# Kernel optimization log

Hardware: AMD Instinct MI355X
Metric: run time of the kernel (lower is better)

The kernel has to match this reference:

```python
import jax, jax.numpy as jnp
import numpy as np

B, C, H, W = 8, 256, 80, 80
NH, NP = 8, 4               # num_heads, num_points
CPH = C // NH               # channels per head


def conv1x1(x, w, b):
    # x: [B,Cin,H,W], w: [Cout,Cin], b: [Cout]
    return jnp.einsum('bchw,oc->bohw', x, w) + b[None, :, None, None]


def grid_sample_bilinear(img, grid):
    # img: [N,C,Hi,Wi], grid: [N,Hg,Wg,2] in [-1,1] (x,y), align_corners=True, zeros padding
    N, Cc, Hi, Wi = img.shape
    Hg, Wg = grid.shape[1], grid.shape[2]
    ix = (grid[..., 0] + 1.0) * 0.5 * (Wi - 1)
    iy = (grid[..., 1] + 1.0) * 0.5 * (Hi - 1)
    x0 = jnp.floor(ix); y0 = jnp.floor(iy)
    x1 = x0 + 1.0;      y1 = y0 + 1.0
    wx1 = ix - x0; wx0 = 1.0 - wx1
    wy1 = iy - y0; wy0 = 1.0 - wy1
    imf = img.reshape(N, Cc, Hi * Wi)

    def gather(xc, yc):
        valid = (xc >= 0) & (xc <= Wi - 1) & (yc >= 0) & (yc <= Hi - 1)
        xi = jnp.clip(xc, 0, Wi - 1).astype(jnp.int32)
        yi = jnp.clip(yc, 0, Hi - 1).astype(jnp.int32)
        idx = (yi * Wi + xi).reshape(N, 1, Hg * Wg)
        v = jnp.take_along_axis(imf, jnp.broadcast_to(idx, (N, Cc, Hg * Wg)), axis=2)
        v = v.reshape(N, Cc, Hg, Wg)
        return v * valid[:, None].astype(img.dtype)

    out = (gather(x0, y0) * (wx0 * wy0)[:, None]
           + gather(x1, y0) * (wx1 * wy0)[:, None]
           + gather(x0, y1) * (wx0 * wy1)[:, None]
           + gather(x1, y1) * (wx1 * wy1)[:, None])
    return out


def setup_inputs() -> dict:
    key = jax.random.key(0)
    ks = jax.random.split(key, 9)
    s = 1.0 / np.sqrt(C)
    x = jax.random.normal(ks[0], (B, C, H, W), dtype=jnp.float32)
    Wv = jax.random.normal(ks[1], (C, C), dtype=jnp.float32) * s
    bv = jnp.zeros((C,), dtype=jnp.float32)
    Woff = jax.random.normal(ks[2], (NH * NP * 2, C), dtype=jnp.float32) * 0.01
    boff = jax.random.normal(ks[3], (NH * NP * 2,), dtype=jnp.float32) * 0.01
    Wa = jax.random.normal(ks[4], (NH * NP, C), dtype=jnp.float32) * 0.01
    ba = jnp.full((NH * NP,), float(np.log(1.0 / NP)), dtype=jnp.float32)
    Wo = jax.random.normal(ks[5], (C, C), dtype=jnp.float32) * s
    bo = jnp.zeros((C,), dtype=jnp.float32)
    return {"x": x, "Wv": Wv, "bv": bv, "Woff": Woff, "boff": boff,
            "Wa": Wa, "ba": ba, "Wo": Wo, "bo": bo}


def reference(x, Wv, bv, Woff, boff, Wa, ba, Wo, bo):
    value = conv1x1(x, Wv, bv)                      # [B,C,H,W]
    offsets = conv1x1(x, Woff, boff)                # [B,NH*NP*2,H,W]
    attn = conv1x1(x, Wa, ba).reshape(B, NH, NP, H, W)
    attn = jax.nn.softmax(attn, axis=2)             # softmax over points

    gy, gx = jnp.meshgrid(jnp.linspace(-1.0, 1.0, H), jnp.linspace(-1.0, 1.0, W), indexing='ij')
    base_grid = jnp.stack((gx, gy), axis=-1)[None, None, None]          # [1,1,1,H,W,2]

    off = offsets.reshape(B, NH, NP, 2, H, W).transpose(0, 1, 2, 4, 5, 3)  # [B,NH,NP,H,W,2]
    grid = (base_grid + off).reshape(B * NH * NP, H, W, 2)

    v = value.reshape(B, NH, CPH, H, W)
    v = jnp.broadcast_to(v[:, :, None], (B, NH, NP, CPH, H, W)).reshape(B * NH * NP, CPH, H, W)

    sampled = grid_sample_bilinear(v, grid).reshape(B, NH, NP, CPH, H, W)
    weighted = (sampled * attn[:, :, :, None]).sum(axis=2)              # [B,NH,CPH,H,W]
    weighted = weighted.reshape(B, C, H, W)
    return conv1x1(weighted, Wo, bo) + x
```

## Files before the change

kernel.cpp:

```cpp
#include <hip/hip_runtime.h>
#include <cstddef>
#include <cstdint>

#define B_    8
#define C_    256
#define Himg  80
#define Wimg  80
#define HW_   6400
#define NH_   8
#define NP_   4
#define MPROJ 352

using bf16x8 = __attribute__((ext_vector_type(8))) short;
using f32x4  = __attribute__((ext_vector_type(4))) float;
using f16x8  = __attribute__((ext_vector_type(8))) _Float16;
using f16x4  = __attribute__((ext_vector_type(4))) _Float16;

__device__ __forceinline__ unsigned short f2bf(float f) {
    union { float f; uint32_t u; } v; v.f = f;
    uint32_t r = v.u + 0x7FFFu + ((v.u >> 16) & 1u);
    return (unsigned short)(r >> 16);
}
__device__ __forceinline__ float bf2f(unsigned short s) {
    union { uint32_t u; float f; } v; v.u = ((uint32_t)s) << 16;
    return v.f;
}

#define GLD16(gsrc, ldst) \
    __builtin_amdgcn_global_load_lds( \
        (const __attribute__((address_space(1))) unsigned int*)(gsrc), \
        (__attribute__((address_space(3))) unsigned int*)(ldst), 16, 0, 0)

__global__ __launch_bounds__(256) void prep_and_transpose(
        const float* __restrict__ Wv,  const float* __restrict__ bv,
        const float* __restrict__ Woff, const float* __restrict__ boff,
        const float* __restrict__ Wa,  const float* __restrict__ ba,
        const float* __restrict__ Wo,  const float* __restrict__ x,
        short* __restrict__ WcatBf, short* __restrict__ WoBf,
        float* __restrict__ bcat,   short* __restrict__ xT) {
    __shared__ float tile[64][68];
    const int bid = blockIdx.x;
    const int t = threadIdx.x;
    if (bid < 640) {
        int o = bid;
        if (o < 384) {
            const float* src = nullptr; float bias = 0.f;
            if (o < 256)      { src = Wv   + (size_t)o * 256;         bias = bv[o];         }
            else if (o < 320) { src = Woff + (size_t)(o - 256) * 256; bias = boff[o - 256]; }
            else if (o < 352) { src = Wa   + (size_t)(o - 320) * 256; bias = ba[o - 320];   }
            WcatBf[(size_t)o * 256 + t] = src ? (short)f2bf(src[t]) : (short)0;
            if (t == 0) bcat[o] = bias;
        } else {
            int oo = o - 384;
            WoBf[(size_t)oo * 256 + t] = (short)f2bf(Wo[(size_t)oo * 256 + t]);
        }
        return;
    }
    const int b2 = bid - 640;
    const int p0 = (b2 % 100) * 64;
    const int k0 = ((b2 / 100) & 3) * 64;
    const int b  = b2 / 400;
    const float* xb = x + ((size_t)b * C_ + k0) * HW_ + p0;
    #pragma unroll
    for (int r = 0; r < 4; ++r) {
        int kk = r * 16 + (t >> 4);
        int pp = (t & 15) * 4;
        float4 v = *(const float4*)(xb + (size_t)kk * HW_ + pp);
        *(float4*)&tile[kk][pp] = v;
    }
    __syncthreads();
    const int pp = t >> 2, kc = (t & 3) * 16;
    short tmp[16];
    #pragma unroll
    for (int i = 0; i < 16; ++i) tmp[i] = (short)f2bf(tile[kc + i][pp]);
    short* dst = xT + ((size_t)b * HW_ + p0 + pp) * 256 + k0 + kc;
    *(bf16x8*)dst       = *(bf16x8*)tmp;
    *(bf16x8*)(dst + 8) = *(bf16x8*)(tmp + 8);
}

#define PSTAGE(buf, k0)                                                         \
    _Pragma("unroll")                                                           \
    for (int q = 0; q < 4; ++q) {                                               \
        int i = wid * 4 + q;                                                    \
        int row = i * 8 + (lane >> 3);                                          \
        int sc  = (lane & 7) ^ (row & 7);                                       \
        GLD16(Wb  + (size_t)(o0 + row) * 256 + (k0) + sc * 8,                   \
              &lA[(buf)][i * 512]);                                             \
        GLD16(xTb + (size_t)(p0 + row) * 256 + (k0) + sc * 8,                   \
              &lB[(buf)][i * 512]);                                             \
    }

#define PCOMPUTE(buf)                                                           \
    _Pragma("unroll")                                                           \
    for (int kk = 0; kk < 2; ++kk) {                                            \
        bf16x8 af[4], bfr[4];                                                   \
        _Pragma("unroll")                                                       \
        for (int m = 0; m < 4; ++m) {                                           \
            int row = wo0 + m * 16 + (lane & 15);                               \
            int cph = (kk * 4 + (lane >> 4)) ^ (row & 7);                       \
            af[m] = *(const bf16x8*)&lA[(buf)][row * 64 + cph * 8];             \
        }                                                                       \
        _Pragma("unroll")                                                       \
        for (int nn = 0; nn < 4; ++nn) {                                        \
            int row = wp0 + nn * 16 + (lane & 15);                              \
            int cph = (kk * 4 + (lane >> 4)) ^ (row & 7);                       \
            bfr[nn] = *(const bf16x8*)&lB[(buf)][row * 64 + cph * 8];           \
        }                                                                       \
        _Pragma("unroll")                                                       \
        for (int m = 0; m < 4; ++m)                                             \
            _Pragma("unroll")                                                   \
            for (int nn = 0; nn < 4; ++nn)                                      \
                acc[m][nn] = __builtin_amdgcn_mfma_f32_16x16x32_bf16(           \
                    af[m], bfr[nn], acc[m][nn], 0, 0, 0);                       \
    }

__global__ __launch_bounds__(256) void gemm_proj_mfma(
        const short* __restrict__ Wb, const float* __restrict__ bcat,
        const short* __restrict__ xT,
        short* __restrict__ val, _Float16* __restrict__ meta) {
    __shared__ short lA[2][8192];
    __shared__ short lB[2][8192];
    const int n = blockIdx.x;
    const int w = (n & 7) * 150 + (n >> 3);
    const int b = w / 150;
    const int r150 = w % 150;
    const int o0 = (r150 % 3) * 128;
    const int p0 = (r150 / 3) * 128;
    const int t = threadIdx.x;
    const int wid = t >> 6, lane = t & 63;
    const int wo0 = (wid & 1) * 64, wp0 = (wid >> 1) * 64;
    const short* xTb = xT + (size_t)b * HW_ * 256;
    f32x4 acc[4][4] = {};

    PSTAGE(0, 0)
    #pragma unroll
    for (int kt = 0; kt < 4; ++kt) {
        const int cur = kt & 1;
        if (kt > 0) __builtin_amdgcn_s_barrier();
        if (kt < 3) { PSTAGE(cur ^ 1, (kt + 1) * 64) }
        if (kt < 3) { asm volatile("s_waitcnt vmcnt(8)" ::: "memory"); }
        else        { asm volatile("s_waitcnt vmcnt(0)" ::: "memory"); }
        __builtin_amdgcn_sched_barrier(0);
        __builtin_amdgcn_s_barrier();
        PCOMPUTE(cur)
    }

    #pragma unroll
    for (int m = 0; m < 4; ++m) {
        int oc = o0 + wo0 + m * 16 + (lane >> 4) * 4;
        if (oc >= MPROJ) continue;
        float4 bias = *(const float4*)(bcat + oc);
        #pragma unroll
        for (int nn = 0; nn < 4; ++nn) {
            int p = p0 + wp0 + nn * 16 + (lane & 15);
            f32x4 a = acc[m][nn];
            float v0 = a[0] + bias.x, v1 = a[1] + bias.y;
            float v2 = a[2] + bias.z, v3 = a[3] + bias.w;
            if (oc < 256) {
                int h = oc >> 5, c0 = oc & 31;
                ushort4 u;
                u.x = f2bf(v0); u.y = f2bf(v1); u.z = f2bf(v2); u.w = f2bf(v3);
                *(ushort4*)(val + (((size_t)(b * NH_ + h) * HW_) + p) * 32 + c0) = u;
            } else if (oc < 320) {
                f16x4 f;
                f[0] = (_Float16)(v0 * 39.5f); f[1] = (_Float16)(v1 * 39.5f);
                f[2] = (_Float16)(v2 * 39.5f); f[3] = (_Float16)(v3 * 39.5f);
                *(f16x4*)(meta + ((size_t)b * HW_ + p) * 96 + (oc - 256)) = f;
            } else {
                float mx = fmaxf(fmaxf(v0, v1), fmaxf(v2, v3));
                float e0 = __expf(v0 - mx), e1 = __expf(v1 - mx);
                float e2 = __expf(v2 - mx), e3 = __expf(v3 - mx);
                float inv = 1.f / (e0 + e1 + e2 + e3);
                f16x4 f;
                f[0] = (_Float16)(e0 * inv); f[1] = (_Float16)(e1 * inv);
                f[2] = (_Float16)(e2 * inv); f[3] = (_Float16)(e3 * inv);
                *(f16x4*)(meta + ((size_t)b * HW_ + p) * 96 + (oc - 256)) = f;
            }
        }
    }
}

__global__ __launch_bounds__(256) void sample_kern(
        const short* __restrict__ val, const _Float16* __restrict__ meta,
        short* __restrict__ wout) {
    const int t = threadIdx.x;
    const int wid = t >> 6, lane = t & 63;
    const int sub = lane >> 5, li = lane & 31;
    const int h = li >> 2, j = li & 3;
    const int orig = blockIdx.x;
    const int b = orig & 7;
    const int p = (orig >> 3) * 8 + wid * 2 + sub;
    const int yy = p / Wimg;
    const int xx = p - yy * Wimg;

    const _Float16* mrow = meta + ((size_t)b * HW_ + p) * 96;
    f16x4 w4 = *(const f16x4*)(mrow + 64 + h * 4);
    float wgt[4] = {(float)w4[0], (float)w4[1], (float)w4[2], (float)w4[3]};

    f16x8 off8 = *(const f16x8*)(mrow + h * 8);
    float ox[4] = {(float)off8[0], (float)off8[2], (float)off8[4], (float)off8[6]};
    float oy[4] = {(float)off8[1], (float)off8[3], (float)off8[5], (float)off8[7]};

    const short* vb = val + ((size_t)(b * NH_ + h) * HW_) * 32 + j * 8;

    float acc[8] = {};
    #pragma unroll
    for (int pt = 0; pt < NP_; ++pt) {
        float ix = (float)xx + ox[pt];
        float iy = (float)yy + oy[pt];
        float x0f = floorf(ix), y0f = floorf(iy);
        int   x0  = (int)x0f,   y0  = (int)y0f;
        float wx1 = ix - x0f, wx0 = 1.f - wx1;
        float wy1 = iy - y0f, wy0 = 1.f - wy1;
        int x0c = min(max(x0, 0), Wimg - 1), x1c = min(max(x0 + 1, 0), Wimg - 1);
        int y0c = min(max(y0, 0), Himg - 1), y1c = min(max(y0 + 1, 0), Himg - 1);
        float vx0 = (x0 >= 0 && x0 <= Wimg - 1)         ? wx0 : 0.f;
        float vx1 = (x0 + 1 >= 0 && x0 + 1 <= Wimg - 1) ? wx1 : 0.f;
        float vy0 = (y0 >= 0 && y0 <= Himg - 1)         ? wy0 : 0.f;
        float vy1 = (y0 + 1 >= 0 && y0 + 1 <= Himg - 1) ? wy1 : 0.f;
        bf16x8 u00 = *(const bf16x8*)(vb + (size_t)(y0c * Wimg + x0c) * 32);
        bf16x8 u01 = *(const bf16x8*)(vb + (size_t)(y0c * Wimg + x1c) * 32);
        bf16x8 u10 = *(const bf16x8*)(vb + (size_t)(y1c * Wimg + x0c) * 32);
        bf16x8 u11 = *(const bf16x8*)(vb + (size_t)(y1c * Wimg + x1c) * 32);
        float w00 = vy0 * vx0 * wgt[pt], w01 = vy0 * vx1 * wgt[pt];
        float w10 = vy1 * vx0 * wgt[pt], w11 = vy1 * vx1 * wgt[pt];
        #pragma unroll
        for (int c = 0; c < 8; ++c) {
            acc[c] += w00 * bf2f((unsigned short)u00[c])
                    + w01 * bf2f((unsigned short)u01[c])
                    + w10 * bf2f((unsigned short)u10[c])
                    + w11 * bf2f((unsigned short)u11[c]);
        }
    }
    short tmp[8];
    #pragma unroll
    for (int c = 0; c < 8; ++c) tmp[c] = (short)f2bf(acc[c]);
    *(bf16x8*)(wout + ((size_t)b * HW_ + p) * 256 + h * 32 + j * 8) = *(bf16x8*)tmp;
}

#define OSTAGE(buf, k0)                                                         \
    _Pragma("unroll")                                                           \
    for (int q = 0; q < 2; ++q) {                                               \
        int i = wid * 2 + q;                                                    \
        int row = i * 8 + (lane >> 3);                                          \
        int sc  = (lane & 7) ^ (row & 7);                                       \
        GLD16(Wb + (size_t)(o0 + row) * 256 + (k0) + sc * 8,                    \
              &lA[(buf)][i * 512]);                                             \
    }                                                                           \
    _Pragma("unroll")                                                           \
    for (int q = 0; q < 4; ++q) {                                               \
        int i = wid * 4 + q;                                                    \
        int row = i * 8 + (lane >> 3);                                          \
        int sc  = (lane & 7) ^ (row & 7);                                       \
        GLD16(wgtb + (size_t)(p0 + row) * 256 + (k0) + sc * 8,                  \
              &lB[(buf)][i * 512]);                                             \
    }

#define OCOMPUTE(buf)                                                           \
    _Pragma("unroll")                                                           \
    for (int kk = 0; kk < 2; ++kk) {                                            \
        bf16x8 af[4], bfr[2];                                                   \
        _Pragma("unroll")                                                       \
        for (int m = 0; m < 4; ++m) {                                           \
            int row = m * 16 + (lane & 15);                                     \
            int cph = (kk * 4 + (lane >> 4)) ^ (row & 7);                       \
            af[m] = *(const bf16x8*)&lA[(buf)][row * 64 + cph * 8];             \
        }                                                                       \
        _Pragma("unroll")                                                       \
        for (int nn = 0; nn < 2; ++nn) {                                        \
            int row = wid * 32 + nn * 16 + (lane & 15);                         \
            int cph = (kk * 4 + (lane >> 4)) ^ (row & 7);                       \
            bfr[nn] = *(const bf16x8*)&lB[(buf)][row * 64 + cph * 8];           \
        }                                                                       \
        _Pragma("unroll")                                                       \
        for (int m = 0; m < 4; ++m)                                             \
            _Pragma("unroll")                                                   \
            for (int nn = 0; nn < 2; ++nn)                                      \
                acc[m][nn] = __builtin_amdgcn_mfma_f32_16x16x32_bf16(           \
                    af[m], bfr[nn], acc[m][nn], 0, 0, 0);                       \
    }

__global__ __launch_bounds__(256) void gemm_out_mfma(
        const short* __restrict__ Wb, const float* __restrict__ bo,
        const short* __restrict__ wgt, const float* __restrict__ x,
        float* __restrict__ out) {
    __shared__ short lA[2][4096];
    __shared__ short lB[2][8192];
    const int n = blockIdx.x;
    const int w = (n & 7) * 200 + (n >> 3);
    const int b = w / 200;
    const int r200 = w % 200;
    const int o0 = (r200 % 4) * 64;
    const int p0 = (r200 / 4) * 128;
    const int t = threadIdx.x;
    const int wid = t >> 6, lane = t & 63;
    const short* wgtb = wgt + (size_t)b * HW_ * 256;
    f32x4 acc[4][2] = {};

    OSTAGE(0, 0)
    #pragma unroll
    for (int kt = 0; kt < 4; ++kt) {
        const int cur = kt & 1;
        if (kt > 0) __builtin_amdgcn_s_barrier();
        if (kt < 3) { OSTAGE(cur ^ 1, (kt + 1) * 64) }
        if (kt < 3) { asm volatile("s_waitcnt vmcnt(6)" ::: "memory"); }
        else        { asm volatile("s_waitcnt vmcnt(0)" ::: "memory"); }
        __builtin_amdgcn_sched_barrier(0);
        __builtin_amdgcn_s_barrier();
        OCOMPUTE(cur)
    }

    #pragma unroll
    for (int m = 0; m < 4; ++m) {
        int oc = o0 + m * 16 + (lane >> 4) * 4;
        float4 bias = *(const float4*)(bo + oc);
        float br[4] = {bias.x, bias.y, bias.z, bias.w};
        #pragma unroll
        for (int nn = 0; nn < 2; ++nn) {
            int p = p0 + wid * 32 + nn * 16 + (lane & 15);
            f32x4 a = acc[m][nn];
            #pragma unroll
            for (int reg = 0; reg < 4; ++reg) {
                size_t ad = ((size_t)b * C_ + oc + reg) * HW_ + p;
                out[ad] = a[reg] + br[reg] + x[ad];
            }
        }
    }
}

extern "C" void kernel_launch(void* const* d_in, const int* in_sizes, int n_in,
                              void* d_out, int out_size, void* d_ws, size_t ws_size,
                              hipStream_t stream) {
    const float* x    = (const float*)d_in[0];
    const float* Wv   = (const float*)d_in[1];
    const float* bv   = (const float*)d_in[2];
    const float* Woff = (const float*)d_in[3];
    const float* boff = (const float*)d_in[4];
    const float* Wa   = (const float*)d_in[5];
    const float* ba   = (const float*)d_in[6];
    const float* Wo   = (const float*)d_in[7];
    const float* bo   = (const float*)d_in[8];
    float* out = (float*)d_out;
    char* base = (char*)d_ws;

    short*    WcatBf = (short*)(base);
    short*    WoBf   = (short*)(base + 196608);
    float*    bcat   = (float*)(base + 327680);
    short*    xT     = (short*)(base + 329728);
    short*    val    = (short*)(base + 26544128);
    _Float16* meta   = (_Float16*)(base + 52758528);
    short*    wbuf   = (short*)(base + 72419328);

    prep_and_transpose<<<dim3(3840), dim3(256), 0, stream>>>(
        Wv, bv, Woff, boff, Wa, ba, Wo, x, WcatBf, WoBf, bcat, xT);
    gemm_proj_mfma<<<dim3(1200), dim3(256), 0, stream>>>(WcatBf, bcat, xT, val, meta);
    sample_kern<<<dim3(6400), dim3(256), 0, stream>>>(val, meta, wbuf);
    gemm_out_mfma<<<dim3(1600), dim3(256), 0, stream>>>(WoBf, bo, wbuf, x, out);
}
```

Baseline: 91.13 us.

## Split bilinear corners across lane pairs in sampler and prioritize MFMA waves

The sampling kernel now gives each pair of lanes one channel group, with each lane loading the two corners in its own x column. The two partial sums are then combined with a shuffle, which halves the per-thread gather loads and doubles the grid size to add latency hiding. Separately, both GEMM kernels raise wave priority around their MFMA bursts with s_setprio, so that matrix issue is favoured over other waves' loads. The cost is twice as many threads and blocks in the sampler, plus an extra cross-lane reduction.

```diff
diff --git a/kernel.cpp b/kernel.cpp
--- a/kernel.cpp
+++ b/kernel.cpp
@@ -106,12 +106,14 @@
             int cph = (kk * 4 + (lane >> 4)) ^ (row & 7);                       \
             bfr[nn] = *(const bf16x8*)&lB[(buf)][row * 64 + cph * 8];           \
         }                                                                       \
+        __builtin_amdgcn_s_setprio(1);                                          \
         _Pragma("unroll")                                                       \
         for (int m = 0; m < 4; ++m)                                             \
             _Pragma("unroll")                                                   \
             for (int nn = 0; nn < 4; ++nn)                                      \
                 acc[m][nn] = __builtin_amdgcn_mfma_f32_16x16x32_bf16(           \
                     af[m], bfr[nn], acc[m][nn], 0, 0, 0);                       \
+        __builtin_amdgcn_s_setprio(0);                                          \
     }
 
 __global__ __launch_bounds__(256) void gemm_proj_mfma(
@@ -185,23 +187,24 @@
         short* __restrict__ wout) {
     const int t = threadIdx.x;
     const int wid = t >> 6, lane = t & 63;
-    const int sub = lane >> 5, li = lane & 31;
-    const int h = li >> 2, j = li & 3;
+    const int h  = lane >> 3;
+    const int r  = lane & 7;
+    const int cg = r >> 1;
+    const int s  = r & 1;
     const int orig = blockIdx.x;
     const int b = orig & 7;
-    const int p = (orig >> 3) * 8 + wid * 2 + sub;
+    const int p = (orig >> 3) * 4 + wid;
     const int yy = p / Wimg;
     const int xx = p - yy * Wimg;
 
     const _Float16* mrow = meta + ((size_t)b * HW_ + p) * 96;
     f16x4 w4 = *(const f16x4*)(mrow + 64 + h * 4);
     float wgt[4] = {(float)w4[0], (float)w4[1], (float)w4[2], (float)w4[3]};
-
     f16x8 off8 = *(const f16x8*)(mrow + h * 8);
     float ox[4] = {(float)off8[0], (float)off8[2], (float)off8[4], (float)off8[6]};
     float oy[4] = {(float)off8[1], (float)off8[3], (float)off8[5], (float)off8[7]};
 
-    const short* vb = val + ((size_t)(b * NH_ + h) * HW_) * 32 + j * 8;
+    const short* vb = val + ((size_t)(b * NH_ + h) * HW_) * 32 + cg * 8;
 
     float acc[8] = {};
     #pragma unroll
@@ -212,30 +215,30 @@
         int   x0  = (int)x0f,   y0  = (int)y0f;
         float wx1 = ix - x0f, wx0 = 1.f - wx1;
         float wy1 = iy - y0f, wy0 = 1.f - wy1;
-        int x0c = min(max(x0, 0), Wimg - 1), x1c = min(max(x0 + 1, 0), Wimg - 1);
+        int xs = x0 + s;
+        int xc = min(max(xs, 0), Wimg - 1);
         int y0c = min(max(y0, 0), Himg - 1), y1c = min(max(y0 + 1, 0), Himg - 1);
-        float vx0 = (x0 >= 0 && x0 <= Wimg - 1)         ? wx0 : 0.f;
-        float vx1 = (x0 + 1 >= 0 && x0 + 1 <= Wimg - 1) ? wx1 : 0.f;
+        float vxs = s ? wx1 : wx0;
+        vxs = (xs >= 0 && xs <= Wimg - 1) ? vxs : 0.f;
         float vy0 = (y0 >= 0 && y0 <= Himg - 1)         ? wy0 : 0.f;
         float vy1 = (y0 + 1 >= 0 && y0 + 1 <= Himg - 1) ? wy1 : 0.f;
-        bf16x8 u00 = *(const bf16x8*)(vb + (size_t)(y0c * Wimg + x0c) * 32);
-        bf16x8 u01 = *(const bf16x8*)(vb + (size_t)(y0c * Wimg + x1c) * 32);
-        bf16x8 u10 = *(const bf16x8*)(vb + (size_t)(y1c * Wimg + x0c) * 32);
-        bf16x8 u11 = *(const bf16x8*)(vb + (size_t)(y1c * Wimg + x1c) * 32);
-        float w00 = vy0 * vx0 * wgt[pt], w01 = vy0 * vx1 * wgt[pt];
-        float w10 = vy1 * vx0 * wgt[pt], w11 = vy1 * vx1 * wgt[pt];
+        bf16x8 u0 = *(const bf16x8*)(vb + (size_t)(y0c * Wimg + xc) * 32);
+        bf16x8 u1 = *(const bf16x8*)(vb + (size_t)(y1c * Wimg + xc) * 32);
+        float wA = vy0 * vxs * wgt[pt], wB = vy1 * vxs * wgt[pt];
         #pragma unroll
-        for (int c = 0; c < 8; ++c) {
-            acc[c] += w00 * bf2f((unsigned short)u00[c])
-                    + w01 * bf2f((unsigned short)u01[c])
-                    + w10 * bf2f((unsigned short)u10[c])
-                    + w11 * bf2f((unsigned short)u11[c]);
-        }
-    }
-    short tmp[8];
-    #pragma unroll
-    for (int c = 0; c < 8; ++c) tmp[c] = (short)f2bf(acc[c]);
-    *(bf16x8*)(wout + ((size_t)b * HW_ + p) * 256 + h * 32 + j * 8) = *(bf16x8*)tmp;
+        for (int c = 0; c < 8; ++c)
+            acc[c] += wA * bf2f((unsigned short)u0[c])
+                    + wB * bf2f((unsigned short)u1[c]);
+    }
+    #pragma unroll
+    for (int c = 0; c < 8; ++c)
+        acc[c] += __shfl_xor(acc[c], 1);
+    if (s == 0) {
+        short tmp[8];
+        #pragma unroll
+        for (int c = 0; c < 8; ++c) tmp[c] = (short)f2bf(acc[c]);
+        *(bf16x8*)(wout + ((size_t)b * HW_ + p) * 256 + h * 32 + cg * 8) = *(bf16x8*)tmp;
+    }
 }
 
 #define OSTAGE(buf, k0)                                                         \
@@ -272,12 +275,14 @@
             int cph = (kk * 4 + (lane >> 4)) ^ (row & 7);                       \
             bfr[nn] = *(const bf16x8*)&lB[(buf)][row * 64 + cph * 8];           \
         }                                                                       \
+        __builtin_amdgcn_s_setprio(1);                                          \
         _Pragma("unroll")                                                       \
         for (int m = 0; m < 4; ++m)                                             \
             _Pragma("unroll")                                                   \
             for (int nn = 0; nn < 2; ++nn)                                      \
                 acc[m][nn] = __builtin_amdgcn_mfma_f32_16x16x32_bf16(           \
                     af[m], bfr[nn], acc[m][nn], 0, 0, 0);                       \
+        __builtin_amdgcn_s_setprio(0);                                          \
     }
 
 __global__ __launch_bounds__(256) void gemm_out_mfma(
@@ -354,6 +359,6 @@
     prep_and_transpose<<<dim3(3840), dim3(256), 0, stream>>>(
         Wv, bv, Woff, boff, Wa, ba, Wo, x, WcatBf, WoBf, bcat, xT);
     gemm_proj_mfma<<<dim3(1200), dim3(256), 0, stream>>>(WcatBf, bcat, xT, val, meta);
-    sample_kern<<<dim3(6400), dim3(256), 0, stream>>>(val, meta, wbuf);
+    sample_kern<<<dim3(12800), dim3(256), 0, stream>>>(val, meta, wbuf);
     gemm_out_mfma<<<dim3(1600), dim3(256), 0, stream>>>(WoBf, bo, wbuf, x, out);
 }
```

New measurement: 92.27 us. No clear change (+1.2%).

## Fuse x transpose and bf16 conversion into projection GEMM B-operand staging

Applied to the files above, without the earlier changes.

Removes the separate transpose pass that wrote a bf16 transposed copy of x to workspace. The projection GEMM now loads fp32 x directly, converts it to bf16 in registers and writes it swizzled into LDS, with a register prefetch overlapping the MFMA compute. This eliminates an intermediate write and read of x, but the B operand no longer uses async global-to-LDS loads, each output tile re-reads fp32 x, and extra block syncs are added.

```diff
diff --git a/kernel.cpp b/kernel.cpp
--- a/kernel.cpp
+++ b/kernel.cpp
@@ -31,63 +31,52 @@
         (const __attribute__((address_space(1))) unsigned int*)(gsrc), \
         (__attribute__((address_space(3))) unsigned int*)(ldst), 16, 0, 0)
 
-__global__ __launch_bounds__(256) void prep_and_transpose(
+__global__ __launch_bounds__(256) void prep_w(
         const float* __restrict__ Wv,  const float* __restrict__ bv,
         const float* __restrict__ Woff, const float* __restrict__ boff,
         const float* __restrict__ Wa,  const float* __restrict__ ba,
-        const float* __restrict__ Wo,  const float* __restrict__ x,
+        const float* __restrict__ Wo,
         short* __restrict__ WcatBf, short* __restrict__ WoBf,
-        float* __restrict__ bcat,   short* __restrict__ xT) {
-    __shared__ float tile[64][68];
-    const int bid = blockIdx.x;
-    const int t = threadIdx.x;
-    if (bid < 640) {
-        int o = bid;
-        if (o < 384) {
-            const float* src = nullptr; float bias = 0.f;
-            if (o < 256)      { src = Wv   + (size_t)o * 256;         bias = bv[o];         }
-            else if (o < 320) { src = Woff + (size_t)(o - 256) * 256; bias = boff[o - 256]; }
-            else if (o < 352) { src = Wa   + (size_t)(o - 320) * 256; bias = ba[o - 320];   }
-            WcatBf[(size_t)o * 256 + t] = src ? (short)f2bf(src[t]) : (short)0;
-            if (t == 0) bcat[o] = bias;
-        } else {
-            int oo = o - 384;
-            WoBf[(size_t)oo * 256 + t] = (short)f2bf(Wo[(size_t)oo * 256 + t]);
-        }
-        return;
-    }
-    const int b2 = bid - 640;
-    const int p0 = (b2 % 100) * 64;
-    const int k0 = ((b2 / 100) & 3) * 64;
-    const int b  = b2 / 400;
-    const float* xb = x + ((size_t)b * C_ + k0) * HW_ + p0;
-    #pragma unroll
-    for (int r = 0; r < 4; ++r) {
-        int kk = r * 16 + (t >> 4);
-        int pp = (t & 15) * 4;
-        float4 v = *(const float4*)(xb + (size_t)kk * HW_ + pp);
-        *(float4*)&tile[kk][pp] = v;
-    }
-    __syncthreads();
-    const int pp = t >> 2, kc = (t & 3) * 16;
-    short tmp[16];
-    #pragma unroll
-    for (int i = 0; i < 16; ++i) tmp[i] = (short)f2bf(tile[kc + i][pp]);
-    short* dst = xT + ((size_t)b * HW_ + p0 + pp) * 256 + k0 + kc;
-    *(bf16x8*)dst       = *(bf16x8*)tmp;
-    *(bf16x8*)(dst + 8) = *(bf16x8*)(tmp + 8);
-}
-
-#define PSTAGE(buf, k0)                                                         \
+        float* __restrict__ bcat) {
+    int o = blockIdx.x, t = threadIdx.x;
+    if (o < 384) {
+        const float* src = nullptr; float bias = 0.f;
+        if (o < 256)      { src = Wv   + (size_t)o * 256;         bias = bv[o];         }
+        else if (o < 320) { src = Woff + (size_t)(o - 256) * 256; bias = boff[o - 256]; }
+        else if (o < 352) { src = Wa   + (size_t)(o - 320) * 256; bias = ba[o - 320];   }
+        WcatBf[(size_t)o * 256 + t] = src ? (short)f2bf(src[t]) : (short)0;
+        if (t == 0) bcat[o] = bias;
+    } else {
+        int oo = o - 384;
+        WoBf[(size_t)oo * 256 + t] = (short)f2bf(Wo[(size_t)oo * 256 + t]);
+    }
+}
+
+#define PASTAGE(buf, k0)                                                        \
     _Pragma("unroll")                                                           \
     for (int q = 0; q < 4; ++q) {                                               \
         int i = wid * 4 + q;                                                    \
         int row = i * 8 + (lane >> 3);                                          \
         int sc  = (lane & 7) ^ (row & 7);                                       \
-        GLD16(Wb  + (size_t)(o0 + row) * 256 + (k0) + sc * 8,                   \
+        GLD16(Wb + (size_t)(o0 + row) * 256 + (k0) + sc * 8,                    \
               &lA[(buf)][i * 512]);                                             \
-        GLD16(xTb + (size_t)(p0 + row) * 256 + (k0) + sc * 8,                   \
-              &lB[(buf)][i * 512]);                                             \
+    }
+
+#define PBLOAD(k0)                                                              \
+    _Pragma("unroll")                                                           \
+    for (int j = 0; j < 8; ++j)                                                 \
+        xv[j] = *(const float4*)(xb + (size_t)((k0) + koct * 8 + j) * HW_);
+
+#define PBWRITE(buf)                                                            \
+    _Pragma("unroll")                                                           \
+    for (int pi = 0; pi < 4; ++pi) {                                            \
+        int p = bp + pi;                                                        \
+        short tmp[8];                                                           \
+        _Pragma("unroll")                                                       \
+        for (int j = 0; j < 8; ++j)                                             \
+            tmp[j] = (short)f2bf(((const float*)&xv[j])[pi]);                   \
+        int phys = koct ^ (p & 7);                                              \
+        *(bf16x8*)&lB[(buf)][p * 64 + phys * 8] = *(bf16x8*)tmp;                \
     }
 
 #define PCOMPUTE(buf)                                                           \
@@ -116,7 +105,7 @@
 
 __global__ __launch_bounds__(256) void gemm_proj_mfma(
         const short* __restrict__ Wb, const float* __restrict__ bcat,
-        const short* __restrict__ xT,
+        const float* __restrict__ x,
         short* __restrict__ val, _Float16* __restrict__ meta) {
     __shared__ short lA[2][8192];
     __shared__ short lB[2][8192];
@@ -129,20 +118,26 @@
     const int t = threadIdx.x;
     const int wid = t >> 6, lane = t & 63;
     const int wo0 = (wid & 1) * 64, wp0 = (wid >> 1) * 64;
-    const short* xTb = xT + (size_t)b * HW_ * 256;
+    const int koct = t >> 5;
+    const int bp   = (t & 31) * 4;
+    const float* xb = x + (size_t)b * C_ * HW_ + p0 + bp;
+    float4 xv[8];
     f32x4 acc[4][4] = {};
 
-    PSTAGE(0, 0)
+    PASTAGE(0, 0)
+    PBLOAD(0)
+    PBWRITE(0)
+    __syncthreads();
+
     #pragma unroll
     for (int kt = 0; kt < 4; ++kt) {
         const int cur = kt & 1;
-        if (kt > 0) __builtin_amdgcn_s_barrier();
-        if (kt < 3) { PSTAGE(cur ^ 1, (kt + 1) * 64) }
-        if (kt < 3) { asm volatile("s_waitcnt vmcnt(8)" ::: "memory"); }
-        else        { asm volatile("s_waitcnt vmcnt(0)" ::: "memory"); }
-        __builtin_amdgcn_sched_barrier(0);
-        __builtin_amdgcn_s_barrier();
+        if (kt < 3) { PASTAGE(cur ^ 1, (kt + 1) * 64) PBLOAD((kt + 1) * 64) }
         PCOMPUTE(cur)
+        if (kt < 3) {
+            PBWRITE(cur ^ 1)
+            __syncthreads();
+        }
     }
 
     #pragma unroll
@@ -346,14 +341,13 @@
     short*    WcatBf = (short*)(base);
     short*    WoBf   = (short*)(base + 196608);
     float*    bcat   = (float*)(base + 327680);
-    short*    xT     = (short*)(base + 329728);
-    short*    val    = (short*)(base + 26544128);
-    _Float16* meta   = (_Float16*)(base + 52758528);
-    short*    wbuf   = (short*)(base + 72419328);
-
-    prep_and_transpose<<<dim3(3840), dim3(256), 0, stream>>>(
-        Wv, bv, Woff, boff, Wa, ba, Wo, x, WcatBf, WoBf, bcat, xT);
-    gemm_proj_mfma<<<dim3(1200), dim3(256), 0, stream>>>(WcatBf, bcat, xT, val, meta);
+    short*    val    = (short*)(base + 329728);
+    _Float16* meta   = (_Float16*)(base + 26544128);
+    short*    wbuf   = (short*)(base + 36374528);
+
+    prep_w<<<dim3(640), dim3(256), 0, stream>>>(Wv, bv, Woff, boff, Wa, ba, Wo,
+                                                WcatBf, WoBf, bcat);
+    gemm_proj_mfma<<<dim3(1200), dim3(256), 0, stream>>>(WcatBf, bcat, x, val, meta);
     sample_kern<<<dim3(6400), dim3(256), 0, stream>>>(val, meta, wbuf);
     gemm_out_mfma<<<dim3(1600), dim3(256), 0, stream>>>(WoBf, bo, wbuf, x, out);
 }
```

After: 91.14 us. Within noise of the previous version (+0.0%).
